# Optimization experiments

Measured on AMD Instinct MI355X. Metric: run time of the kernel, lower is better.

Reference implementation:

```python
import jax, jax.numpy as jnp
import numpy as np

NUM_SRC = 200000
NUM_DST = 100000
NUM_EDGES = 1600000
IN_DIM = 128
HID = 256
OUT_DIM = 128


def layer_norm(h, g, b, eps=1e-5):
    mu = jnp.mean(h, axis=-1, keepdims=True)
    var = jnp.mean((h - mu) ** 2, axis=-1, keepdims=True)
    return (h - mu) * jax.lax.rsqrt(var + eps) * g + b


def setup_inputs() -> dict:
    key = jax.random.key(0)
    ks = jax.random.split(key, 8)
    s_in = 1.0 / np.sqrt(IN_DIM)
    s_hid = 1.0 / np.sqrt(HID)
    return {
        "x": jax.random.normal(ks[0], (NUM_SRC, IN_DIM), dtype=jnp.float32),
        "w_l": jax.random.normal(ks[1], (IN_DIM, HID), dtype=jnp.float32) * s_in,
        "b_l": jnp.zeros((HID,), dtype=jnp.float32),
        "w_r": jax.random.normal(ks[2], (IN_DIM, HID), dtype=jnp.float32) * s_in,
        "ln1_g": jnp.ones((HID,), dtype=jnp.float32),
        "ln1_b": jnp.zeros((HID,), dtype=jnp.float32),
        "w_out": jax.random.normal(ks[3], (HID, OUT_DIM), dtype=jnp.float32) * s_hid,
        "b_out": jnp.zeros((OUT_DIM,), dtype=jnp.float32),
        "ln2_g": jnp.ones((OUT_DIM,), dtype=jnp.float32),
        "ln2_b": jnp.zeros((OUT_DIM,), dtype=jnp.float32),
        "edge_src": jax.random.randint(ks[4], (NUM_EDGES,), 0, NUM_SRC, dtype=jnp.int64),
        "edge_dst": jax.random.randint(ks[5], (NUM_EDGES,), 0, NUM_DST, dtype=jnp.int64),
    }


def reference(x, w_l, b_l, w_r, ln1_g, ln1_b, w_out, b_out, ln2_g, ln2_b, edge_src, edge_dst):
    # SAGEConv bipartite: targets are the first NUM_DST rows of x
    x_tgt = x[:NUM_DST]
    # mean aggregation of source-node messages at destination nodes
    msgs = x[edge_src]  # [E, IN_DIM] irregular gather
    summed = jax.ops.segment_sum(msgs, edge_dst, num_segments=NUM_DST)
    cnt = jax.ops.segment_sum(jnp.ones((NUM_EDGES,), dtype=x.dtype), edge_dst, num_segments=NUM_DST)
    mean_nbr = summed / jnp.maximum(cnt, 1.0)[:, None]
    # out = lin_l(aggr) + lin_r(x_target); dropout p=0 is identity
    h = mean_nbr @ w_l + b_l + x_tgt @ w_r
    h = layer_norm(h, ln1_g, ln1_b)
    h = jax.nn.gelu(h, approximate=False)
    out = h @ w_out + b_out
    out = layer_norm(out, ln2_g, ln2_b)
    return out
```

## Files before the change

### kernel.cpp

```cpp
#include <hip/hip_runtime.h>
#include <math.h>

#define NSRC 200000
#define NDST 100000
#define NEDGE 1600000

typedef unsigned int uint32;
typedef unsigned short u16;

typedef short short8 __attribute__((ext_vector_type(8)));
typedef float f32x4 __attribute__((ext_vector_type(4)));

__device__ __forceinline__ u16 f2b(float f) {
  uint32 u = __float_as_uint(f);
  u += 0x7fffu + ((u >> 16) & 1u);
  return (u16)(u >> 16);
}
__device__ __forceinline__ float b2f_lo(uint32 u) { return __uint_as_float(u << 16); }
__device__ __forceinline__ float b2f_hi(uint32 u) { return __uint_as_float(u & 0xffff0000u); }

#define NBKT 1563
#define BKTCAP 1344
#define NB_H 256
#define EPH (NEDGE / NB_H)
#define NB_W 384
#define NB_CVT 25000

__global__ __launch_bounds__(256) void k_prep(const float* __restrict__ x, u16* __restrict__ xb,
                                              const float* __restrict__ wl,
                                              const float* __restrict__ wr,
                                              const float* __restrict__ wo,
                                              u16* __restrict__ wp1f, u16* __restrict__ wp2f,
                                              const int do_cvt, const int* __restrict__ src,
                                              const int* __restrict__ dst,
                                              int* __restrict__ bktcnt,
                                              int* __restrict__ pairs) {
  __shared__ int hist[NBKT];
  __shared__ int loff[NBKT];
  if (blockIdx.x < NB_H) {
    int base = blockIdx.x * EPH;
    for (int i = threadIdx.x; i < NBKT; i += 256) hist[i] = 0;
    __syncthreads();
    for (int i = threadIdx.x; i < EPH; i += 256) atomicAdd(&hist[dst[base + i] >> 6], 1);
    __syncthreads();
    for (int i = threadIdx.x; i < NBKT; i += 256) {
      int h = hist[i];
      loff[i] = h ? atomicAdd(&bktcnt[i * 16], h) : 0;
      hist[i] = 0;
    }
    __syncthreads();
    for (int i = threadIdx.x; i < EPH; i += 256) {
      int d = dst[base + i];
      int s = src[base + i];
      int bin = d >> 6;
      int r = atomicAdd(&hist[bin], 1);
      int pos = loff[bin] + r;
      if (pos < BKTCAP) pairs[(size_t)bin * BKTCAP + pos] = (s << 6) | (d & 63);
    }
    return;
  }
  int bid = blockIdx.x - NB_H;
  if (bid < NB_W) {
    int t = bid * 256 + threadIdx.x;
    if (t < 65536) {
      int j = t & 7, lane = (t >> 3) & 63, nt = (t >> 9) & 3, kc = (t >> 11) & 7, w = t >> 14;
      int k = kc * 32 + (lane >> 4) * 8 + j;
      int n = w * 64 + nt * 16 + (lane & 15);
      float v = (k < 128) ? wl[k * 256 + n] : wr[(k - 128) * 256 + n];
      wp1f[t] = f2b(v);
    } else {
      int t2 = t - 65536;
      int j = t2 & 7, lane = (t2 >> 3) & 63, nt = (t2 >> 9) & 1, kc = (t2 >> 10) & 7, w = t2 >> 13;
      int k = kc * 32 + (lane >> 4) * 8 + j;
      int n = w * 32 + nt * 16 + (lane & 15);
      wp2f[t2] = f2b(wo[k * 128 + n]);
    }
    return;
  }
  if (!do_cvt) return;
  int idx = (bid - NB_W) * 256 + threadIdx.x;
  size_t i = (size_t)idx * 4;
  if (i < (size_t)NSRC * 128) {
    float4 f = *(const float4*)(x + i);
    uint2 o;
    o.x = (uint32)f2b(f.x) | ((uint32)f2b(f.y) << 16);
    o.y = (uint32)f2b(f.z) | ((uint32)f2b(f.w) << 16);
    *(uint2*)(xb + i) = o;
  }
}

#define LDAH 264
#define LCSR_LD 65

__global__ __launch_bounds__(1024, 8) void k_fused(
    const u16* __restrict__ xb, const float* __restrict__ xf, const int x_is_bf16,
    const int* __restrict__ pairs, const int* __restrict__ bktcnt,
    const u16* __restrict__ wp1f, const u16* __restrict__ wp2f,
    const float* __restrict__ bl_g, const float* __restrict__ g1_g, const float* __restrict__ b1_g,
    const float* __restrict__ bo_g, const float* __restrict__ g2_g, const float* __restrict__ b2_g,
    float* __restrict__ out) {
  __shared__ __align__(16) u16 AH_lds[64 * LDAH];
  __shared__ float2 stats[16][16];
  __shared__ float2 stats2[64];
  __shared__ int lcnt[64];
  __shared__ int lcsr[64 * LCSR_LD];

  const int tid = threadIdx.x;
  const int wave = tid >> 6;
  const int lane = tid & 63;
  const int l15 = lane & 15;
  const int q = lane >> 4;
  const int wr = wave >> 2;
  const int wc = wave & 3;
  const int row0 = blockIdx.x * 64;

  {
    const int bkt = blockIdx.x;
    int total = bktcnt[(size_t)bkt * 16];
    int mp = total < BKTCAP ? total : BKTCAP;
    if (tid < 64) lcnt[tid] = 0;
    __syncthreads();
    for (int i = tid; i < mp; i += 1024) {
      int v = pairs[(size_t)bkt * BKTCAP + i];
      int d6 = v & 63;
      int p = atomicAdd(&lcnt[d6], 1);
      if (p < 64) lcsr[d6 * LCSR_LD + p] = v >> 6;
    }
    __syncthreads();
  }

  {
    const int sub = tid & 15;
    const int r = tid >> 4;
    const int d = row0 + r;
    u16* rowp = AH_lds + r * LDAH;
    if (d < NDST) {
      int n = lcnt[r];
      int m = n < 64 ? n : 64;
      const int* cp = lcsr + r * LCSR_LD;
      float a[8] = {0, 0, 0, 0, 0, 0, 0, 0};
      if (x_is_bf16) {
        int i = 0;
        for (; i + 3 < m; i += 4) {
          uint4 p[4];
#pragma unroll
          for (int u = 0; u < 4; u++)
            p[u] = *(const uint4*)(xb + (size_t)cp[i + u] * 128 + sub * 8);
#pragma unroll
          for (int u = 0; u < 4; u++) {
            a[0] += b2f_lo(p[u].x); a[1] += b2f_hi(p[u].x);
            a[2] += b2f_lo(p[u].y); a[3] += b2f_hi(p[u].y);
            a[4] += b2f_lo(p[u].z); a[5] += b2f_hi(p[u].z);
            a[6] += b2f_lo(p[u].w); a[7] += b2f_hi(p[u].w);
          }
        }
        for (; i < m; i++) {
          uint4 p = *(const uint4*)(xb + (size_t)cp[i] * 128 + sub * 8);
          a[0] += b2f_lo(p.x); a[1] += b2f_hi(p.x);
          a[2] += b2f_lo(p.y); a[3] += b2f_hi(p.y);
          a[4] += b2f_lo(p.z); a[5] += b2f_hi(p.z);
          a[6] += b2f_lo(p.w); a[7] += b2f_hi(p.w);
        }
      } else {
        for (int i = 0; i < m; i++) {
          int s = cp[i];
          const float* p = xf + (size_t)s * 128 + sub * 8;
          float4 f0 = *(const float4*)p;
          float4 f1 = *(const float4*)(p + 4);
          a[0] += f0.x; a[1] += f0.y; a[2] += f0.z; a[3] += f0.w;
          a[4] += f1.x; a[5] += f1.y; a[6] += f1.z; a[7] += f1.w;
        }
      }
      float sc = 1.f / (float)(n > 0 ? n : 1);
      uint4 o;
      o.x = (uint32)f2b(a[0] * sc) | ((uint32)f2b(a[1] * sc) << 16);
      o.y = (uint32)f2b(a[2] * sc) | ((uint32)f2b(a[3] * sc) << 16);
      o.z = (uint32)f2b(a[4] * sc) | ((uint32)f2b(a[5] * sc) << 16);
      o.w = (uint32)f2b(a[6] * sc) | ((uint32)f2b(a[7] * sc) << 16);
      *(uint4*)(rowp + sub * 8) = o;
      uint4 xv;
      if (x_is_bf16) {
        xv = *(const uint4*)(xb + (size_t)d * 128 + sub * 8);
      } else {
        const float* p = xf + (size_t)d * 128 + sub * 8;
        float4 f0 = *(const float4*)p;
        float4 f1 = *(const float4*)(p + 4);
        xv.x = (uint32)f2b(f0.x) | ((uint32)f2b(f0.y) << 16);
        xv.y = (uint32)f2b(f0.z) | ((uint32)f2b(f0.w) << 16);
        xv.z = (uint32)f2b(f1.x) | ((uint32)f2b(f1.y) << 16);
        xv.w = (uint32)f2b(f1.z) | ((uint32)f2b(f1.w) << 16);
      }
      *(uint4*)(rowp + 128 + sub * 8) = xv;
    } else {
      uint4 z = {0u, 0u, 0u, 0u};
      *(uint4*)(rowp + sub * 8) = z;
      *(uint4*)(rowp + 128 + sub * 8) = z;
    }
  }
  __syncthreads();

  f32x4 acc[4];
#pragma unroll
  for (int j = 0; j < 4; j++) acc[j] = (f32x4){0.f, 0.f, 0.f, 0.f};

#pragma unroll 1
  for (int kc = 0; kc < 8; kc++) {
    short8 bfr[4];
    const uint4* bsrc = (const uint4*)(wp1f + (((size_t)wc * 8 + kc) * 4) * 512);
#pragma unroll
    for (int nt = 0; nt < 4; nt++) bfr[nt] = ((const short8*)(bsrc + nt * 64))[lane];
    short8 af = *(const short8*)(AH_lds + (16 * wr + l15) * LDAH + kc * 32 + q * 8);
#pragma unroll
    for (int nt = 0; nt < 4; nt++)
      acc[nt] = __builtin_amdgcn_mfma_f32_16x16x32_bf16(af, bfr[nt], acc[nt], 0, 0, 0);
  }

  float bl[4], g1[4], b1[4];
#pragma unroll
  for (int nt = 0; nt < 4; nt++) {
    int c = 64 * wc + 16 * nt + l15;
    bl[nt] = bl_g[c]; g1[nt] = g1_g[c]; b1[nt] = b1_g[c];
  }
#pragma unroll
  for (int nt = 0; nt < 4; nt++)
#pragma unroll
    for (int r = 0; r < 4; r++) acc[nt][r] += bl[nt];

#pragma unroll
  for (int r = 0; r < 4; r++) {
    float s = 0.f, s2 = 0.f;
#pragma unroll
    for (int nt = 0; nt < 4; nt++) { float v = acc[nt][r]; s += v; s2 += v * v; }
#pragma unroll
    for (int m = 1; m < 16; m <<= 1) { s += __shfl_xor(s, m, 64); s2 += __shfl_xor(s2, m, 64); }
    if (l15 == 0) stats[wave][4 * q + r] = make_float2(s, s2);
  }
  __syncthreads();
  if (tid < 64) {
    int wr_ = tid >> 4, rl = tid & 15;
    float S = 0.f, Q = 0.f;
#pragma unroll
    for (int w = 0; w < 4; w++) { float2 t = stats[wr_ * 4 + w][rl]; S += t.x; Q += t.y; }
    float mu = S * (1.f / 256.f);
    float var = Q * (1.f / 256.f) - mu * mu;
    stats2[tid] = make_float2(mu, rsqrtf(var + 1e-5f));
  }
  __syncthreads();
#pragma unroll
  for (int r = 0; r < 4; r++) {
    int row = 16 * wr + 4 * q + r;
    float2 st = stats2[row];
#pragma unroll
    for (int nt = 0; nt < 4; nt++) {
      float v = acc[nt][r];
      float hn = (v - st.x) * st.y * g1[nt] + b1[nt];
      float t2 = hn * hn;
      float u = fmaf(0.044715f * t2, hn, hn);
      float ge = hn / (1.f + __expf(-1.5957691216f * u));
      AH_lds[row * LDAH + 64 * wc + 16 * nt + l15] = f2b(ge);
    }
  }
  __syncthreads();

  f32x4 acc2[2];
#pragma unroll
  for (int j = 0; j < 2; j++) acc2[j] = (f32x4){0.f, 0.f, 0.f, 0.f};

#pragma unroll 1
  for (int kc = 0; kc < 8; kc++) {
    short8 bfr[2];
    const uint4* bsrc = (const uint4*)(wp2f + (((size_t)wc * 8 + kc) * 2) * 512);
#pragma unroll
    for (int nt = 0; nt < 2; nt++) bfr[nt] = ((const short8*)(bsrc + nt * 64))[lane];
    short8 af = *(const short8*)(AH_lds + (16 * wr + l15) * LDAH + kc * 32 + q * 8);
#pragma unroll
    for (int nt = 0; nt < 2; nt++)
      acc2[nt] = __builtin_amdgcn_mfma_f32_16x16x32_bf16(af, bfr[nt], acc2[nt], 0, 0, 0);
  }

  float bo[2], g2[2], b2c[2];
#pragma unroll
  for (int nt = 0; nt < 2; nt++) {
    int c = 32 * wc + 16 * nt + l15;
    bo[nt] = bo_g[c]; g2[nt] = g2_g[c]; b2c[nt] = b2_g[c];
  }
#pragma unroll
  for (int nt = 0; nt < 2; nt++)
#pragma unroll
    for (int r = 0; r < 4; r++) acc2[nt][r] += bo[nt];

#pragma unroll
  for (int r = 0; r < 4; r++) {
    float s = 0.f, s2 = 0.f;
#pragma unroll
    for (int nt = 0; nt < 2; nt++) { float v = acc2[nt][r]; s += v; s2 += v * v; }
#pragma unroll
    for (int m = 1; m < 16; m <<= 1) { s += __shfl_xor(s, m, 64); s2 += __shfl_xor(s2, m, 64); }
    if (l15 == 0) stats[wave][4 * q + r] = make_float2(s, s2);
  }
  __syncthreads();
  if (tid < 64) {
    int wr_ = tid >> 4, rl = tid & 15;
    float S = 0.f, Q = 0.f;
#pragma unroll
    for (int w = 0; w < 4; w++) { float2 t = stats[wr_ * 4 + w][rl]; S += t.x; Q += t.y; }
    float mu = S * (1.f / 128.f);
    float var = Q * (1.f / 128.f) - mu * mu;
    stats2[tid] = make_float2(mu, rsqrtf(var + 1e-5f));
  }
  __syncthreads();
#pragma unroll
  for (int r = 0; r < 4; r++) {
    int row = 16 * wr + 4 * q + r;
    int R = row0 + row;
    if (R < NDST) {
      float2 st = stats2[row];
#pragma unroll
      for (int nt = 0; nt < 2; nt++) {
        float v = acc2[nt][r];
        out[(size_t)R * 128 + 32 * wc + 16 * nt + l15] = (v - st.x) * st.y * g2[nt] + b2c[nt];
      }
    }
  }
}

extern "C" void kernel_launch(void* const* d_in, const int* in_sizes, int n_in,
                              void* d_out, int out_size, void* d_ws, size_t ws_size,
                              hipStream_t stream) {
  const float* x   = (const float*)d_in[0];
  const float* w_l = (const float*)d_in[1];
  const float* b_l = (const float*)d_in[2];
  const float* w_r = (const float*)d_in[3];
  const float* g1  = (const float*)d_in[4];
  const float* b1  = (const float*)d_in[5];
  const float* w_o = (const float*)d_in[6];
  const float* b_o = (const float*)d_in[7];
  const float* g2  = (const float*)d_in[8];
  const float* b2  = (const float*)d_in[9];
  const int* esrc  = (const int*)d_in[10];
  const int* edst  = (const int*)d_in[11];
  float* out = (float*)d_out;

  char* ws = (char*)d_ws;
  size_t off = 0;
  auto alloc = [&](size_t bytes) -> void* {
    off = (off + 255) & ~(size_t)255;
    void* p = ws + off;
    off += bytes;
    return p;
  };
  int* bktcnt = (int*)alloc((size_t)NBKT * 16 * 4);
  u16* wp1f   = (u16*)alloc((size_t)65536 * 2);
  u16* wp2f   = (u16*)alloc((size_t)32768 * 2);
  int* pairs  = (int*)alloc((size_t)NBKT * BKTCAP * 4);

  size_t rem = (ws_size > off + 512) ? (ws_size - off - 512) : 0;
  size_t xb_bytes = (size_t)NSRC * 128 * 2;
  int x_is_bf16 = (rem >= xb_bytes) ? 1 : 0;
  u16* xb = x_is_bf16 ? (u16*)alloc(xb_bytes) : nullptr;

  hipMemsetAsync(bktcnt, 0, (size_t)NBKT * 16 * 4, stream);
  k_prep<<<NB_H + NB_W + NB_CVT, 256, 0, stream>>>(x, xb, w_l, w_r, w_o, wp1f, wp2f,
                                                   x_is_bf16, esrc, edst, bktcnt, pairs);
  k_fused<<<NBKT, 1024, 0, stream>>>(xb, x, x_is_bf16, pairs, bktcnt, wp1f, wp2f,
                                     b_l, g1, b1, b_o, g2, b2, out);
}
```

Before: 348.2 us.

## Merge prep and fused stages into one persistent cooperative kernel with grid syncs

Replaces the memset, the prep kernel and the fused kernel with a single cooperative persistent kernel. It zeroes the counters, bucket-sorts edges, packs weights and converts x to bf16 using an atomic work counter, then grid-syncs and loops over destination tiles. The goal is to remove launch overhead and the gaps between dependent kernels. In exchange, each block now handles many tiles with 1024 threads and only a few blocks per CU, grid.sync adds cost, and the fused phase gets less parallelism than the original one-block-per-bucket launch.

```diff
diff --git a/kernel.cpp b/kernel.cpp
--- a/kernel.cpp
+++ b/kernel.cpp
@@ -1,5 +1,8 @@
 #include <hip/hip_runtime.h>
+#include <hip/hip_cooperative_groups.h>
 #include <math.h>
+
+namespace cg = cooperative_groups;
 
 #define NSRC 200000
 #define NDST 100000
@@ -21,110 +24,50 @@
 
 #define NBKT 1563
 #define BKTCAP 1344
-#define NB_H 256
-#define EPH (NEDGE / NB_H)
-#define NB_W 384
-#define NB_CVT 25000
-
-__global__ __launch_bounds__(256) void k_prep(const float* __restrict__ x, u16* __restrict__ xb,
-                                              const float* __restrict__ wl,
-                                              const float* __restrict__ wr,
-                                              const float* __restrict__ wo,
-                                              u16* __restrict__ wp1f, u16* __restrict__ wp2f,
-                                              const int do_cvt, const int* __restrict__ src,
-                                              const int* __restrict__ dst,
-                                              int* __restrict__ bktcnt,
-                                              int* __restrict__ pairs) {
-  __shared__ int hist[NBKT];
-  __shared__ int loff[NBKT];
-  if (blockIdx.x < NB_H) {
-    int base = blockIdx.x * EPH;
-    for (int i = threadIdx.x; i < NBKT; i += 256) hist[i] = 0;
-    __syncthreads();
-    for (int i = threadIdx.x; i < EPH; i += 256) atomicAdd(&hist[dst[base + i] >> 6], 1);
-    __syncthreads();
-    for (int i = threadIdx.x; i < NBKT; i += 256) {
-      int h = hist[i];
-      loff[i] = h ? atomicAdd(&bktcnt[i * 16], h) : 0;
-      hist[i] = 0;
-    }
-    __syncthreads();
-    for (int i = threadIdx.x; i < EPH; i += 256) {
-      int d = dst[base + i];
-      int s = src[base + i];
-      int bin = d >> 6;
-      int r = atomicAdd(&hist[bin], 1);
-      int pos = loff[bin] + r;
-      if (pos < BKTCAP) pairs[(size_t)bin * BKTCAP + pos] = (s << 6) | (d & 63);
-    }
-    return;
-  }
-  int bid = blockIdx.x - NB_H;
-  if (bid < NB_W) {
-    int t = bid * 256 + threadIdx.x;
-    if (t < 65536) {
-      int j = t & 7, lane = (t >> 3) & 63, nt = (t >> 9) & 3, kc = (t >> 11) & 7, w = t >> 14;
-      int k = kc * 32 + (lane >> 4) * 8 + j;
-      int n = w * 64 + nt * 16 + (lane & 15);
-      float v = (k < 128) ? wl[k * 256 + n] : wr[(k - 128) * 256 + n];
-      wp1f[t] = f2b(v);
-    } else {
-      int t2 = t - 65536;
-      int j = t2 & 7, lane = (t2 >> 3) & 63, nt = (t2 >> 9) & 1, kc = (t2 >> 10) & 7, w = t2 >> 13;
-      int k = kc * 32 + (lane >> 4) * 8 + j;
-      int n = w * 32 + nt * 16 + (lane & 15);
-      wp2f[t2] = f2b(wo[k * 128 + n]);
-    }
-    return;
-  }
-  if (!do_cvt) return;
-  int idx = (bid - NB_W) * 256 + threadIdx.x;
-  size_t i = (size_t)idx * 4;
-  if (i < (size_t)NSRC * 128) {
-    float4 f = *(const float4*)(x + i);
-    uint2 o;
-    o.x = (uint32)f2b(f.x) | ((uint32)f2b(f.y) << 16);
-    o.y = (uint32)f2b(f.z) | ((uint32)f2b(f.w) << 16);
-    *(uint2*)(xb + i) = o;
-  }
-}
-
+#define NB_SORT 256
+#define EPH (NEDGE / NB_SORT)
+#define NCVT_CHUNK 6250
+#define NPREP_CHUNK 96
 #define LDAH 264
 #define LCSR_LD 65
 
-__global__ __launch_bounds__(1024, 8) void k_fused(
-    const u16* __restrict__ xb, const float* __restrict__ xf, const int x_is_bf16,
-    const int* __restrict__ pairs, const int* __restrict__ bktcnt,
-    const u16* __restrict__ wp1f, const u16* __restrict__ wp2f,
-    const float* __restrict__ bl_g, const float* __restrict__ g1_g, const float* __restrict__ b1_g,
-    const float* __restrict__ bo_g, const float* __restrict__ g2_g, const float* __restrict__ b2_g,
-    float* __restrict__ out) {
-  __shared__ __align__(16) u16 AH_lds[64 * LDAH];
-  __shared__ float2 stats[16][16];
-  __shared__ float2 stats2[64];
-  __shared__ int lcnt[64];
-  __shared__ int lcsr[64 * LCSR_LD];
-
-  const int tid = threadIdx.x;
+struct KArgs {
+  const float* x; u16* xb; int x_is_bf16;
+  const float *wl, *wr, *wo; u16 *wp1f, *wp2f;
+  const int *src, *dst;
+  int *bktcnt, *pairs, *cvt_ctr;
+  const float *bl, *g1, *b1, *bo, *g2, *b2;
+  float* out;
+};
+
+struct FusedSmem {
+  u16 AH[64 * LDAH];
+  float2 stats[16][16];
+  float2 stats2[64];
+  int lcnt[64];
+  int lcsr[64 * LCSR_LD];
+};
+
+__device__ __forceinline__ void fused_tile(FusedSmem& sm, const int tid, const int bkt,
+                                           const KArgs& A) {
   const int wave = tid >> 6;
   const int lane = tid & 63;
   const int l15 = lane & 15;
   const int q = lane >> 4;
   const int wr = wave >> 2;
   const int wc = wave & 3;
-  const int row0 = blockIdx.x * 64;
+  const int row0 = bkt * 64;
 
   {
-    const int bkt = blockIdx.x;
-    int total = bktcnt[(size_t)bkt * 16];
+    int total = A.bktcnt[(size_t)bkt * 16];
     int mp = total < BKTCAP ? total : BKTCAP;
-    if (tid < 64) lcnt[tid] = 0;
+    if (tid < 64) sm.lcnt[tid] = 0;
     __syncthreads();
     for (int i = tid; i < mp; i += 1024) {
-      int v = pairs[(size_t)bkt * BKTCAP + i];
+      int v = A.pairs[(size_t)bkt * BKTCAP + i];
       int d6 = v & 63;
-      int p = atomicAdd(&lcnt[d6], 1);
-      if (p < 64) lcsr[d6 * LCSR_LD + p] = v >> 6;
+      int p = atomicAdd(&sm.lcnt[d6], 1);
+      if (p < 64) sm.lcsr[d6 * LCSR_LD + p] = v >> 6;
     }
     __syncthreads();
   }
@@ -133,19 +76,19 @@
     const int sub = tid & 15;
     const int r = tid >> 4;
     const int d = row0 + r;
-    u16* rowp = AH_lds + r * LDAH;
+    u16* rowp = sm.AH + r * LDAH;
     if (d < NDST) {
-      int n = lcnt[r];
+      int n = sm.lcnt[r];
       int m = n < 64 ? n : 64;
-      const int* cp = lcsr + r * LCSR_LD;
+      const int* cp = sm.lcsr + r * LCSR_LD;
       float a[8] = {0, 0, 0, 0, 0, 0, 0, 0};
-      if (x_is_bf16) {
+      if (A.x_is_bf16) {
         int i = 0;
         for (; i + 3 < m; i += 4) {
           uint4 p[4];
 #pragma unroll
           for (int u = 0; u < 4; u++)
-            p[u] = *(const uint4*)(xb + (size_t)cp[i + u] * 128 + sub * 8);
+            p[u] = *(const uint4*)(A.xb + (size_t)cp[i + u] * 128 + sub * 8);
 #pragma unroll
           for (int u = 0; u < 4; u++) {
             a[0] += b2f_lo(p[u].x); a[1] += b2f_hi(p[u].x);
@@ -155,7 +98,7 @@
           }
         }
         for (; i < m; i++) {
-          uint4 p = *(const uint4*)(xb + (size_t)cp[i] * 128 + sub * 8);
+          uint4 p = *(const uint4*)(A.xb + (size_t)cp[i] * 128 + sub * 8);
           a[0] += b2f_lo(p.x); a[1] += b2f_hi(p.x);
           a[2] += b2f_lo(p.y); a[3] += b2f_hi(p.y);
           a[4] += b2f_lo(p.z); a[5] += b2f_hi(p.z);
@@ -164,7 +107,7 @@
       } else {
         for (int i = 0; i < m; i++) {
           int s = cp[i];
-          const float* p = xf + (size_t)s * 128 + sub * 8;
+          const float* p = A.x + (size_t)s * 128 + sub * 8;
           float4 f0 = *(const float4*)p;
           float4 f1 = *(const float4*)(p + 4);
           a[0] += f0.x; a[1] += f0.y; a[2] += f0.z; a[3] += f0.w;
@@ -179,10 +122,10 @@
       o.w = (uint32)f2b(a[6] * sc) | ((uint32)f2b(a[7] * sc) << 16);
       *(uint4*)(rowp + sub * 8) = o;
       uint4 xv;
-      if (x_is_bf16) {
-        xv = *(const uint4*)(xb + (size_t)d * 128 + sub * 8);
+      if (A.x_is_bf16) {
+        xv = *(const uint4*)(A.xb + (size_t)d * 128 + sub * 8);
       } else {
-        const float* p = xf + (size_t)d * 128 + sub * 8;
+        const float* p = A.x + (size_t)d * 128 + sub * 8;
         float4 f0 = *(const float4*)p;
         float4 f1 = *(const float4*)(p + 4);
         xv.x = (uint32)f2b(f0.x) | ((uint32)f2b(f0.y) << 16);
@@ -202,14 +145,13 @@
   f32x4 acc[4];
 #pragma unroll
   for (int j = 0; j < 4; j++) acc[j] = (f32x4){0.f, 0.f, 0.f, 0.f};
-
 #pragma unroll 1
   for (int kc = 0; kc < 8; kc++) {
     short8 bfr[4];
-    const uint4* bsrc = (const uint4*)(wp1f + (((size_t)wc * 8 + kc) * 4) * 512);
+    const uint4* bsrc = (const uint4*)(A.wp1f + (((size_t)wc * 8 + kc) * 4) * 512);
 #pragma unroll
     for (int nt = 0; nt < 4; nt++) bfr[nt] = ((const short8*)(bsrc + nt * 64))[lane];
-    short8 af = *(const short8*)(AH_lds + (16 * wr + l15) * LDAH + kc * 32 + q * 8);
+    short8 af = *(const short8*)(sm.AH + (16 * wr + l15) * LDAH + kc * 32 + q * 8);
 #pragma unroll
     for (int nt = 0; nt < 4; nt++)
       acc[nt] = __builtin_amdgcn_mfma_f32_16x16x32_bf16(af, bfr[nt], acc[nt], 0, 0, 0);
@@ -219,13 +161,12 @@
 #pragma unroll
   for (int nt = 0; nt < 4; nt++) {
     int c = 64 * wc + 16 * nt + l15;
-    bl[nt] = bl_g[c]; g1[nt] = g1_g[c]; b1[nt] = b1_g[c];
+    bl[nt] = A.bl[c]; g1[nt] = A.g1[c]; b1[nt] = A.b1[c];
   }
 #pragma unroll
   for (int nt = 0; nt < 4; nt++)
 #pragma unroll
     for (int r = 0; r < 4; r++) acc[nt][r] += bl[nt];
-
 #pragma unroll
   for (int r = 0; r < 4; r++) {
     float s = 0.f, s2 = 0.f;
@@ -233,23 +174,23 @@
     for (int nt = 0; nt < 4; nt++) { float v = acc[nt][r]; s += v; s2 += v * v; }
 #pragma unroll
     for (int m = 1; m < 16; m <<= 1) { s += __shfl_xor(s, m, 64); s2 += __shfl_xor(s2, m, 64); }
-    if (l15 == 0) stats[wave][4 * q + r] = make_float2(s, s2);
+    if (l15 == 0) sm.stats[wave][4 * q + r] = make_float2(s, s2);
   }
   __syncthreads();
   if (tid < 64) {
     int wr_ = tid >> 4, rl = tid & 15;
     float S = 0.f, Q = 0.f;
 #pragma unroll
-    for (int w = 0; w < 4; w++) { float2 t = stats[wr_ * 4 + w][rl]; S += t.x; Q += t.y; }
+    for (int w = 0; w < 4; w++) { float2 t = sm.stats[wr_ * 4 + w][rl]; S += t.x; Q += t.y; }
     float mu = S * (1.f / 256.f);
     float var = Q * (1.f / 256.f) - mu * mu;
-    stats2[tid] = make_float2(mu, rsqrtf(var + 1e-5f));
+    sm.stats2[tid] = make_float2(mu, rsqrtf(var + 1e-5f));
   }
   __syncthreads();
 #pragma unroll
   for (int r = 0; r < 4; r++) {
     int row = 16 * wr + 4 * q + r;
-    float2 st = stats2[row];
+    float2 st = sm.stats2[row];
 #pragma unroll
     for (int nt = 0; nt < 4; nt++) {
       float v = acc[nt][r];
@@ -257,7 +198,7 @@
       float t2 = hn * hn;
       float u = fmaf(0.044715f * t2, hn, hn);
       float ge = hn / (1.f + __expf(-1.5957691216f * u));
-      AH_lds[row * LDAH + 64 * wc + 16 * nt + l15] = f2b(ge);
+      sm.AH[row * LDAH + 64 * wc + 16 * nt + l15] = f2b(ge);
     }
   }
   __syncthreads();
@@ -265,14 +206,13 @@
   f32x4 acc2[2];
 #pragma unroll
   for (int j = 0; j < 2; j++) acc2[j] = (f32x4){0.f, 0.f, 0.f, 0.f};
-
 #pragma unroll 1
   for (int kc = 0; kc < 8; kc++) {
     short8 bfr[2];
-    const uint4* bsrc = (const uint4*)(wp2f + (((size_t)wc * 8 + kc) * 2) * 512);
+    const uint4* bsrc = (const uint4*)(A.wp2f + (((size_t)wc * 8 + kc) * 2) * 512);
 #pragma unroll
     for (int nt = 0; nt < 2; nt++) bfr[nt] = ((const short8*)(bsrc + nt * 64))[lane];
-    short8 af = *(const short8*)(AH_lds + (16 * wr + l15) * LDAH + kc * 32 + q * 8);
+    short8 af = *(const short8*)(sm.AH + (16 * wr + l15) * LDAH + kc * 32 + q * 8);
 #pragma unroll
     for (int nt = 0; nt < 2; nt++)
       acc2[nt] = __builtin_amdgcn_mfma_f32_16x16x32_bf16(af, bfr[nt], acc2[nt], 0, 0, 0);
@@ -282,13 +222,12 @@
 #pragma unroll
   for (int nt = 0; nt < 2; nt++) {
     int c = 32 * wc + 16 * nt + l15;
-    bo[nt] = bo_g[c]; g2[nt] = g2_g[c]; b2c[nt] = b2_g[c];
+    bo[nt] = A.bo[c]; g2[nt] = A.g2[c]; b2c[nt] = A.b2[c];
   }
 #pragma unroll
   for (int nt = 0; nt < 2; nt++)
 #pragma unroll
     for (int r = 0; r < 4; r++) acc2[nt][r] += bo[nt];
-
 #pragma unroll
   for (int r = 0; r < 4; r++) {
     float s = 0.f, s2 = 0.f;
@@ -296,17 +235,17 @@
     for (int nt = 0; nt < 2; nt++) { float v = acc2[nt][r]; s += v; s2 += v * v; }
 #pragma unroll
     for (int m = 1; m < 16; m <<= 1) { s += __shfl_xor(s, m, 64); s2 += __shfl_xor(s2, m, 64); }
-    if (l15 == 0) stats[wave][4 * q + r] = make_float2(s, s2);
+    if (l15 == 0) sm.stats[wave][4 * q + r] = make_float2(s, s2);
   }
   __syncthreads();
   if (tid < 64) {
     int wr_ = tid >> 4, rl = tid & 15;
     float S = 0.f, Q = 0.f;
 #pragma unroll
-    for (int w = 0; w < 4; w++) { float2 t = stats[wr_ * 4 + w][rl]; S += t.x; Q += t.y; }
+    for (int w = 0; w < 4; w++) { float2 t = sm.stats[wr_ * 4 + w][rl]; S += t.x; Q += t.y; }
     float mu = S * (1.f / 128.f);
     float var = Q * (1.f / 128.f) - mu * mu;
-    stats2[tid] = make_float2(mu, rsqrtf(var + 1e-5f));
+    sm.stats2[tid] = make_float2(mu, rsqrtf(var + 1e-5f));
   }
   __syncthreads();
 #pragma unroll
@@ -314,14 +253,159 @@
     int row = 16 * wr + 4 * q + r;
     int R = row0 + row;
     if (R < NDST) {
-      float2 st = stats2[row];
+      float2 st = sm.stats2[row];
 #pragma unroll
       for (int nt = 0; nt < 2; nt++) {
         float v = acc2[nt][r];
-        out[(size_t)R * 128 + 32 * wc + 16 * nt + l15] = (v - st.x) * st.y * g2[nt] + b2c[nt];
+        A.out[(size_t)R * 128 + 32 * wc + 16 * nt + l15] = (v - st.x) * st.y * g2[nt] + b2c[nt];
       }
     }
   }
+}
+
+__global__ __launch_bounds__(1024, 8) void k_all(KArgs A) {
+  __shared__ __align__(16) FusedSmem sm;
+  __shared__ int hist[NBKT];
+  __shared__ int loff[NBKT];
+  __shared__ int s_chunk;
+  cg::grid_group grid = cg::this_grid();
+  const int tid = threadIdx.x;
+  const int bid = blockIdx.x;
+  const int nb = gridDim.x;
+
+  for (int i = bid * 1024 + tid; i < NBKT * 16; i += nb * 1024) A.bktcnt[i] = 0;
+  if (bid == 0 && tid == 0) A.cvt_ctr[0] = 0;
+  grid.sync();
+
+  for (int c = bid; c < NB_SORT; c += nb) {
+    int base = c * EPH;
+    for (int i = tid; i < NBKT; i += 1024) hist[i] = 0;
+    __syncthreads();
+    for (int i = tid; i < EPH; i += 1024) atomicAdd(&hist[A.dst[base + i] >> 6], 1);
+    __syncthreads();
+    for (int i = tid; i < NBKT; i += 1024) {
+      int h = hist[i];
+      loff[i] = h ? atomicAdd(&A.bktcnt[i * 16], h) : 0;
+      hist[i] = 0;
+    }
+    __syncthreads();
+    for (int i = tid; i < EPH; i += 1024) {
+      int d = A.dst[base + i];
+      int s = A.src[base + i];
+      int bin = d >> 6;
+      int r = atomicAdd(&hist[bin], 1);
+      int pos = loff[bin] + r;
+      if (pos < BKTCAP) A.pairs[(size_t)bin * BKTCAP + pos] = (s << 6) | (d & 63);
+    }
+    __syncthreads();
+  }
+
+  for (int c = nb - 1 - bid; c < NPREP_CHUNK; c += nb) {
+    int t = c * 1024 + tid;
+    if (t < 65536) {
+      int j = t & 7, lane = (t >> 3) & 63, nt = (t >> 9) & 3, kc = (t >> 11) & 7, w = t >> 14;
+      int k = kc * 32 + (lane >> 4) * 8 + j;
+      int n = w * 64 + nt * 16 + (lane & 15);
+      float v = (k < 128) ? A.wl[k * 256 + n] : A.wr[(k - 128) * 256 + n];
+      A.wp1f[t] = f2b(v);
+    } else {
+      int t2 = t - 65536;
+      int j = t2 & 7, lane = (t2 >> 3) & 63, nt = (t2 >> 9) & 1, kc = (t2 >> 10) & 7, w = t2 >> 13;
+      int k = kc * 32 + (lane >> 4) * 8 + j;
+      int n = w * 32 + nt * 16 + (lane & 15);
+      A.wp2f[t2] = f2b(A.wo[k * 128 + n]);
+    }
+  }
+
+  if (A.x_is_bf16) {
+    for (;;) {
+      if (tid == 0) s_chunk = atomicAdd(A.cvt_ctr, 1);
+      __syncthreads();
+      int c = s_chunk;
+      __syncthreads();
+      if (c >= NCVT_CHUNK) break;
+      size_t i = ((size_t)c * 1024 + tid) * 4;
+      float4 f = *(const float4*)(A.x + i);
+      uint2 o;
+      o.x = (uint32)f2b(f.x) | ((uint32)f2b(f.y) << 16);
+      o.y = (uint32)f2b(f.z) | ((uint32)f2b(f.w) << 16);
+      *(uint2*)(A.xb + i) = o;
+    }
+  }
+  grid.sync();
+
+  for (int bkt = bid; bkt < NBKT; bkt += nb) {
+    fused_tile(sm, tid, bkt, A);
+    __syncthreads();
+  }
+}
+
+__global__ __launch_bounds__(256) void k_prep(const float* __restrict__ x, u16* __restrict__ xb,
+                                              const float* __restrict__ wl,
+                                              const float* __restrict__ wr,
+                                              const float* __restrict__ wo,
+                                              u16* __restrict__ wp1f, u16* __restrict__ wp2f,
+                                              const int do_cvt, const int* __restrict__ src,
+                                              const int* __restrict__ dst,
+                                              int* __restrict__ bktcnt,
+                                              int* __restrict__ pairs) {
+  __shared__ int hist[NBKT];
+  __shared__ int loff[NBKT];
+  if (blockIdx.x < NB_SORT) {
+    int base = blockIdx.x * EPH;
+    for (int i = threadIdx.x; i < NBKT; i += 256) hist[i] = 0;
+    __syncthreads();
+    for (int i = threadIdx.x; i < EPH; i += 256) atomicAdd(&hist[dst[base + i] >> 6], 1);
+    __syncthreads();
+    for (int i = threadIdx.x; i < NBKT; i += 256) {
+      int h = hist[i];
+      loff[i] = h ? atomicAdd(&bktcnt[i * 16], h) : 0;
+      hist[i] = 0;
+    }
+    __syncthreads();
+    for (int i = threadIdx.x; i < EPH; i += 256) {
+      int d = dst[base + i];
+      int s = src[base + i];
+      int bin = d >> 6;
+      int r = atomicAdd(&hist[bin], 1);
+      int pos = loff[bin] + r;
+      if (pos < BKTCAP) pairs[(size_t)bin * BKTCAP + pos] = (s << 6) | (d & 63);
+    }
+    return;
+  }
+  int bid = blockIdx.x - NB_SORT;
+  if (bid < 384) {
+    int t = bid * 256 + threadIdx.x;
+    if (t < 65536) {
+      int j = t & 7, lane = (t >> 3) & 63, nt = (t >> 9) & 3, kc = (t >> 11) & 7, w = t >> 14;
+      int k = kc * 32 + (lane >> 4) * 8 + j;
+      int n = w * 64 + nt * 16 + (lane & 15);
+      float v = (k < 128) ? wl[k * 256 + n] : wr[(k - 128) * 256 + n];
+      wp1f[t] = f2b(v);
+    } else {
+      int t2 = t - 65536;
+      int j = t2 & 7, lane = (t2 >> 3) & 63, nt = (t2 >> 9) & 1, kc = (t2 >> 10) & 7, w = t2 >> 13;
+      int k = kc * 32 + (lane >> 4) * 8 + j;
+      int n = w * 32 + nt * 16 + (lane & 15);
+      wp2f[t2] = f2b(wo[k * 128 + n]);
+    }
+    return;
+  }
+  if (!do_cvt) return;
+  int idx = (bid - 384) * 256 + threadIdx.x;
+  size_t i = (size_t)idx * 4;
+  if (i < (size_t)NSRC * 128) {
+    float4 f = *(const float4*)(x + i);
+    uint2 o;
+    o.x = (uint32)f2b(f.x) | ((uint32)f2b(f.y) << 16);
+    o.y = (uint32)f2b(f.z) | ((uint32)f2b(f.w) << 16);
+    *(uint2*)(xb + i) = o;
+  }
+}
+
+__global__ __launch_bounds__(1024, 8) void k_fused(KArgs A) {
+  __shared__ __align__(16) FusedSmem sm;
+  fused_tile(sm, threadIdx.x, blockIdx.x, A);
 }
 
 extern "C" void kernel_launch(void* const* d_in, const int* in_sizes, int n_in,
@@ -349,19 +433,41 @@
     off += bytes;
     return p;
   };
-  int* bktcnt = (int*)alloc((size_t)NBKT * 16 * 4);
-  u16* wp1f   = (u16*)alloc((size_t)65536 * 2);
-  u16* wp2f   = (u16*)alloc((size_t)32768 * 2);
-  int* pairs  = (int*)alloc((size_t)NBKT * BKTCAP * 4);
+  int* bktcnt  = (int*)alloc((size_t)NBKT * 16 * 4);
+  u16* wp1f    = (u16*)alloc((size_t)65536 * 2);
+  u16* wp2f    = (u16*)alloc((size_t)32768 * 2);
+  int* pairs   = (int*)alloc((size_t)NBKT * BKTCAP * 4);
+  int* cvt_ctr = (int*)alloc(256);
 
   size_t rem = (ws_size > off + 512) ? (ws_size - off - 512) : 0;
   size_t xb_bytes = (size_t)NSRC * 128 * 2;
   int x_is_bf16 = (rem >= xb_bytes) ? 1 : 0;
   u16* xb = x_is_bf16 ? (u16*)alloc(xb_bytes) : nullptr;
 
-  hipMemsetAsync(bktcnt, 0, (size_t)NBKT * 16 * 4, stream);
-  k_prep<<<NB_H + NB_W + NB_CVT, 256, 0, stream>>>(x, xb, w_l, w_r, w_o, wp1f, wp2f,
-                                                   x_is_bf16, esrc, edst, bktcnt, pairs);
-  k_fused<<<NBKT, 1024, 0, stream>>>(xb, x, x_is_bf16, pairs, bktcnt, wp1f, wp2f,
-                                     b_l, g1, b1, b_o, g2, b2, out);
-}
+  KArgs A;
+  A.x = x; A.xb = xb; A.x_is_bf16 = x_is_bf16;
+  A.wl = w_l; A.wr = w_r; A.wo = w_o; A.wp1f = wp1f; A.wp2f = wp2f;
+  A.src = esrc; A.dst = edst;
+  A.bktcnt = bktcnt; A.pairs = pairs; A.cvt_ctr = cvt_ctr;
+  A.bl = b_l; A.g1 = g1; A.b1 = b1; A.bo = b_o; A.g2 = g2; A.b2 = b2;
+  A.out = out;
+
+  int nbpc = 0;
+  hipError_t oe = hipOccupancyMaxActiveBlocksPerMultiprocessor(&nbpc, k_all, 1024, 0);
+  int grid = (oe == hipSuccess && nbpc > 0) ? nbpc * 256 : 0;
+  if (grid > 512) grid = 512;
+  bool ok = false;
+  if (grid >= 64) {
+    void* params[] = { (void*)&A };
+    hipError_t e = hipLaunchCooperativeKernel((const void*)k_all, dim3(grid), dim3(1024),
+                                              params, 0, stream);
+    ok = (e == hipSuccess);
+    if (!ok) (void)hipGetLastError();
+  }
+  if (!ok) {
+    hipMemsetAsync(bktcnt, 0, (size_t)NBKT * 16 * 4, stream);
+    k_prep<<<NB_SORT + 384 + 25000, 256, 0, stream>>>(x, xb, w_l, w_r, w_o, wp1f, wp2f,
+                                                      x_is_bf16, esrc, edst, bktcnt, pairs);
+    k_fused<<<NBKT, 1024, 0, stream>>>(A);
+  }
+}
```

Measured after the change: 579.5 us. +66.4%, slower.
